# Kernel tuning notes

Measured on AMD Instinct MI355X. Metric: run time of the kernel, lower is better.

The kernel has to match this reference:

```python
import jax, jax.numpy as jnp
import numpy as np

TARGET_FIDELITY = 0.95
WEIGHT = 0.1
BATCH, DIM = 8192, 2048


def setup_inputs() -> dict:
    key = jax.random.key(0)
    k1, k2 = jax.random.split(key)
    # Scale by 1/sqrt(DIM) so each row is roughly unit-norm (quantum-state-like)
    # and the trace fidelity lands strictly inside the clamp interval [0, 1].
    scale = 1.0 / np.sqrt(DIM)
    latent_codes = jax.random.normal(k1, (BATCH, DIM), dtype=jnp.float32) * scale
    target_codes = jax.random.normal(k2, (BATCH, DIM), dtype=jnp.float32) * scale
    return {"latent_codes": latent_codes, "target_codes": target_codes}


def reference(latent_codes, target_codes):
    batch = latent_codes.shape[0]
    # rho = mean_i z_i z_i^T  ==  L^T L / B  (single GEMM instead of B outer products)
    rho = jnp.matmul(latent_codes.T, latent_codes) / batch      # [D, D]
    sigma = jnp.matmul(target_codes.T, target_codes) / batch    # [D, D]
    # trace(rho @ sigma) = sum(rho * sigma) since both are symmetric
    fidelity = jnp.clip(jnp.sum(rho * sigma), 0.0, 1.0)
    loss = WEIGHT * jnp.abs(fidelity - TARGET_FIDELITY)
    return loss
```

## Files before the change

kernel.cpp:

```cpp
#include <hip/hip_runtime.h>
#include <stdint.h>

#define BATCH 8192
#define DIM   2048

typedef unsigned char  u8;
typedef unsigned short u16;
typedef unsigned int   u32;

using v8i  = __attribute__((ext_vector_type(8)))  int;
using v16f = __attribute__((ext_vector_type(16))) float;

#if __has_builtin(__builtin_amdgcn_cvt_scalef32_pk_fp4_f32)
#define HW_FP4 1
#endif

__device__ __forceinline__ void gl_lds16(const void* g, void* l) {
  __builtin_amdgcn_global_load_lds(
      (const __attribute__((address_space(1))) u32*)g,
      (__attribute__((address_space(3))) u32*)l, 16, 0, 0);
}

__device__ __forceinline__ u32 nib4(float x) {
  float xs = x * 64.0f;
  float a  = fabsf(xs);
  u32 n = (u32)(a >= 0.25f) + (u32)(a >= 0.75f) + (u32)(a >= 1.25f) +
          (u32)(a >= 1.75f) + (u32)(a >= 2.5f)  + (u32)(a >= 3.5f)  +
          (u32)(a >= 5.0f);
  return n | (xs < 0.0f ? 8u : 0u);
}

__device__ __forceinline__ u16 pack4_fp4(float a, float b, float c, float d) {
#ifdef HW_FP4
  u32 w = __builtin_amdgcn_cvt_scalef32_pk_fp4_f32(0u,  a * 64.0f, b * 64.0f, 1.0f, 0);
  w     = __builtin_amdgcn_cvt_scalef32_pk_fp4_f32(w,   c * 64.0f, d * 64.0f, 1.0f, 1);
  return (u16)w;
#else
  return (u16)(nib4(a) | (nib4(b) << 4) | (nib4(c) << 8) | (nib4(d) << 12));
#endif
}

__global__ __launch_bounds__(256) void tcvt_fp4(
    const float* __restrict__ L, const float* __restrict__ T,
    u8* __restrict__ X, u8* __restrict__ Y,
    float* __restrict__ acc, u32* __restrict__ cnt)
{
  __shared__ u16 ls[64 * 68];

  const int tid = threadIdx.x;
  if (blockIdx.x == 0 && tid == 0) { *acc = 0.0f; *cnt = 0u; }

  int id = blockIdx.x;
  const float* src;
  u8* dst;
  if (id < 1024) { src = L; dst = X; }
  else           { src = T; dst = Y; id -= 1024; }
  const int d0 = (id & 31) * 64;
  const int b0 = (id >> 5) * 256;

  const int s  = tid & 15;
  const int g  = tid >> 4;
  const int sw = s & 12;

  float4 f[4][4];
#pragma unroll
  for (int j = 0; j < 4; ++j)
#pragma unroll
    for (int r = 0; r < 4; ++r)
      f[j][r] = *(const float4*)(src + (size_t)(b0 + j * 64 + g * 4 + r) * DIM
                                 + d0 + s * 4);

#pragma unroll
  for (int j = 0; j < 4; ++j) {
    const int w = (j * 16 + g) ^ sw;
    const float* fp[4] = {(const float*)&f[j][0], (const float*)&f[j][1],
                          (const float*)&f[j][2], (const float*)&f[j][3]};
#pragma unroll
    for (int i = 0; i < 4; ++i)
      ls[(s * 4 + i) * 68 + w] = pack4_fp4(fp[0][i], fp[1][i], fp[2][i], fp[3][i]);
  }
  __syncthreads();

#pragma unroll
  for (int j2 = 0; j2 < 2; ++j2) {
    const int d   = (tid >> 3) + j2 * 32;
    const int o8  = tid & 7;
    const int gsw = (d >> 4) & 3;
    const int g1  = (2 * o8)     ^ gsw;
    const int g2  = (2 * o8 + 1) ^ gsw;
    uint2 a = *(const uint2*)&ls[d * 68 + g1 * 4];
    uint2 b = *(const uint2*)&ls[d * 68 + g2 * 4];
    uint4 v = {a.x, a.y, b.x, b.y};
    *(uint4*)(dst + (size_t)(d0 + d) * (BATCH / 2) + (b0 >> 1) + o8 * 16) = v;
  }
}

__global__ __launch_bounds__(256, 2) void gram_fp4(
    const u8* __restrict__ X, const u8* __restrict__ Y,
    float* __restrict__ Gx, float* __restrict__ Gy)
{
  __shared__ u8 ls[2][2][16384];

  const int tid = threadIdx.x;
  const int bid = blockIdx.x;
  const int t   = bid & 255;
  const u8*  src = (bid < 256) ? X : Y;
  float*     dst = (bid < 256) ? Gx : Gy;
  const int i0  = (t >> 4) * 128;
  const int j0  = (t & 15) * 128;

  const int wave = tid >> 6;
  const int lane = tid & 63;
  const int wr = (wave >> 1) * 64;
  const int wc = (wave & 1) * 64;
  const int lr = lane & 31;
  const int kh = lane >> 5;

  u32 sdst[4], soi[4], soj[4];
#pragma unroll
  for (int rr = 0; rr < 4; ++rr) {
    const int li  = rr * 256 + tid;
    const int row = li >> 3;
    const int p   = li & 7;
    const int gc  = p ^ (row & 7);
    sdst[rr] = (u32)(row * 128 + p * 16);
    soi[rr]  = (u32)(i0 + row) * (BATCH / 2) + gc * 16;
    soj[rr]  = (u32)(j0 + row) * (BATCH / 2) + gc * 16;
  }

  u32 fa[2][4], fb[2][4];
#pragma unroll
  for (int h = 0; h < 2; ++h) {
    const int ra = wr + h * 32 + lr;
    const int rb = wc + h * 32 + lr;
#pragma unroll
    for (int ks = 0; ks < 4; ++ks) {
      const int c = 2 * ks + kh;
      fa[h][ks] = (u32)(ra * 128 + (c ^ (ra & 7)) * 16);
      fb[h][ks] = (u32)(rb * 128 + (c ^ (rb & 7)) * 16);
    }
  }

  v16f acc[2][2] = {};
  const int sc = 0x7F7F7F7F;

#pragma unroll
  for (int rr = 0; rr < 4; ++rr) {
    gl_lds16(src + soi[rr], &ls[0][0][sdst[rr]]);
    gl_lds16(src + soj[rr], &ls[0][1][sdst[rr]]);
  }

  for (int it = 0; it < 32; ++it) {
    __syncthreads();
    const int buf = it & 1;
    if (it < 31) {
      const u32 k1 = (u32)(it + 1) * 128;
#pragma unroll
      for (int rr = 0; rr < 4; ++rr) {
        gl_lds16(src + soi[rr] + k1, &ls[buf ^ 1][0][sdst[rr]]);
        gl_lds16(src + soj[rr] + k1, &ls[buf ^ 1][1][sdst[rr]]);
      }
    }
    const u8* pI = ls[buf][0];
    const u8* pJ = ls[buf][1];
#pragma unroll
    for (int ks = 0; ks < 4; ++ks) {
      v8i a[2], b[2];
#pragma unroll
      for (int h = 0; h < 2; ++h) {
        int4 pa = *(const int4*)&pI[fa[h][ks]];
        a[h] = (v8i){pa.x, pa.y, pa.z, pa.w, 0, 0, 0, 0};
        int4 pb = *(const int4*)&pJ[fb[h][ks]];
        b[h] = (v8i){pb.x, pb.y, pb.z, pb.w, 0, 0, 0, 0};
      }
#pragma unroll
      for (int h = 0; h < 2; ++h)
#pragma unroll
        for (int hc = 0; hc < 2; ++hc)
          acc[h][hc] = __builtin_amdgcn_mfma_scale_f32_32x32x64_f8f6f4(
              a[h], b[hc], acc[h][hc],  4,  4,
              0, sc, 0, sc);
    }
  }

  float4* o = (float4*)(dst + (size_t)t * 16384);
#pragma unroll
  for (int h = 0; h < 2; ++h)
#pragma unroll
    for (int hc = 0; hc < 2; ++hc)
#pragma unroll
      for (int r4 = 0; r4 < 4; ++r4) {
        float4 v = {acc[h][hc][r4 * 4 + 0], acc[h][hc][r4 * 4 + 1],
                    acc[h][hc][r4 * 4 + 2], acc[h][hc][r4 * 4 + 3]};
        o[((h * 2 + hc) * 4 + r4) * 256 + tid] = v;
      }
}

__global__ __launch_bounds__(256) void dot_kernel(
    const float4* __restrict__ Gx, const float4* __restrict__ Gy,
    float* __restrict__ d_acc, u32* __restrict__ d_cnt,
    float* __restrict__ out)
{
  __shared__ float red[4];
  const int tid  = threadIdx.x;
  const int lane = tid & 63;
  const int i0   = blockIdx.x * 256 + tid;
  float s = 0.0f;
#pragma unroll
  for (int j = 0; j < 4; ++j) {
    float4 a = Gx[i0 + j * 262144];
    float4 b = Gy[i0 + j * 262144];
    s += a.x * b.x + a.y * b.y + a.z * b.z + a.w * b.w;
  }
#pragma unroll
  for (int off = 32; off > 0; off >>= 1)
    s += __shfl_down(s, off);
  if (lane == 0) red[tid >> 6] = s;
  __syncthreads();
  if (tid == 0) {
    atomicAdd(d_acc, red[0] + red[1] + red[2] + red[3]);
    __threadfence();
    const u32 old = atomicAdd(d_cnt, 1u);
    if (old == 1023u) {
      float S   = atomicAdd(d_acc, 0.0f);
      float fid = S * 0x1.0p-50f;
      fid = fminf(fmaxf(fid, 0.0f), 1.0f);
      *out = 0.1f * fabsf(fid - 0.95f);
    }
  }
}

extern "C" void kernel_launch(void* const* d_in, const int* in_sizes, int n_in,
                              void* d_out, int out_size, void* d_ws, size_t ws_size,
                              hipStream_t stream) {
  const float* L = (const float*)d_in[0];
  const float* T = (const float*)d_in[1];
  float* out = (float*)d_out;

  const size_t NF4 = (size_t)BATCH * DIM / 2;
  const size_t GEL = (size_t)DIM * DIM;
  u8*    X   = (u8*)d_ws;
  u8*    Y   = (u8*)d_ws + NF4;
  float* Gx  = (float*)((char*)d_ws + 2 * NF4);
  float* Gy  = Gx + GEL;
  float* acc = Gy + GEL;
  u32*   cnt = (u32*)(acc + 1);

  tcvt_fp4<<<2048, 256, 0, stream>>>(L, T, X, Y, acc, cnt);
  gram_fp4<<<512, 256, 0, stream>>>(X, Y, Gx, Gy);
  dot_kernel<<<1024, 256, 0, stream>>>((const float4*)Gx, (const float4*)Gy,
                                       acc, cnt, out);
}
```

Before: 228.3 us.

## Exploit Gram symmetry with triangular tiles and stream-K split across blocks

Only the lower-triangular 128x128 tiles of each Gram matrix are computed: 136 per matrix, 272 in total. Their K iterations are spread evenly over 512 blocks, 17 quanta each, in stream-K style, and partial tiles are combined with float atomicAdd into a zeroed buffer. The dot kernel weights off-diagonal tiles by two, which roughly halves GEMM work and the Gram storage it reads. The costs are many scalar atomics per tile boundary, zeroing the buffer inside the convert kernel, and nondeterministic float summation order. The convert kernel also now double-buffers its input loads.

```diff
diff --git a/kernel.cpp b/kernel.cpp
--- a/kernel.cpp
+++ b/kernel.cpp
@@ -3,13 +3,17 @@
 
 #define BATCH 8192
 #define DIM   2048
+#define NT    272
+#define QTOT  (NT * 32)
+#define QPB   17
 
 typedef unsigned char  u8;
 typedef unsigned short u16;
 typedef unsigned int   u32;
 
-using v8i  = __attribute__((ext_vector_type(8)))  int;
-using v16f = __attribute__((ext_vector_type(16))) float;
+using v8i   = __attribute__((ext_vector_type(8)))  int;
+using v16f  = __attribute__((ext_vector_type(16))) float;
+using f32x4 = __attribute__((ext_vector_type(4)))  float;
 
 #if __has_builtin(__builtin_amdgcn_cvt_scalef32_pk_fp4_f32)
 #define HW_FP4 1
@@ -43,12 +47,18 @@
 __global__ __launch_bounds__(256) void tcvt_fp4(
     const float* __restrict__ L, const float* __restrict__ T,
     u8* __restrict__ X, u8* __restrict__ Y,
-    float* __restrict__ acc, u32* __restrict__ cnt)
+    float* __restrict__ Gc, float* __restrict__ acc, u32* __restrict__ cnt)
 {
   __shared__ u16 ls[64 * 68];
 
   const int tid = threadIdx.x;
   if (blockIdx.x == 0 && tid == 0) { *acc = 0.0f; *cnt = 0u; }
+
+  {
+    const float4 z = {0.f, 0.f, 0.f, 0.f};
+    for (int i = blockIdx.x * 256 + tid; i < NT * 4096; i += 2048 * 256)
+      ((float4*)Gc)[i] = z;
+  }
 
   int id = blockIdx.x;
   const float* src;
@@ -62,22 +72,25 @@
   const int g  = tid >> 4;
   const int sw = s & 12;
 
-  float4 f[4][4];
-#pragma unroll
-  for (int j = 0; j < 4; ++j)
-#pragma unroll
-    for (int r = 0; r < 4; ++r)
-      f[j][r] = *(const float4*)(src + (size_t)(b0 + j * 64 + g * 4 + r) * DIM
-                                 + d0 + s * 4);
+  const float* base = src + (size_t)(b0 + g * 4) * DIM + d0 + s * 4;
+
+  f32x4 f[2][4];
+#pragma unroll
+  for (int r = 0; r < 4; ++r)
+    f[0][r] = *(const f32x4*)(base + (size_t)r * DIM);
 
 #pragma unroll
   for (int j = 0; j < 4; ++j) {
+    if (j < 3) {
+#pragma unroll
+      for (int r = 0; r < 4; ++r)
+        f[(j + 1) & 1][r] = *(const f32x4*)(base + (size_t)((j + 1) * 64 + r) * DIM);
+    }
     const int w = (j * 16 + g) ^ sw;
-    const float* fp[4] = {(const float*)&f[j][0], (const float*)&f[j][1],
-                          (const float*)&f[j][2], (const float*)&f[j][3]};
 #pragma unroll
     for (int i = 0; i < 4; ++i)
-      ls[(s * 4 + i) * 68 + w] = pack4_fp4(fp[0][i], fp[1][i], fp[2][i], fp[3][i]);
+      ls[(s * 4 + i) * 68 + w] =
+          pack4_fp4(f[j & 1][0][i], f[j & 1][1][i], f[j & 1][2][i], f[j & 1][3][i]);
   }
   __syncthreads();
 
@@ -97,17 +110,12 @@
 
 __global__ __launch_bounds__(256, 2) void gram_fp4(
     const u8* __restrict__ X, const u8* __restrict__ Y,
-    float* __restrict__ Gx, float* __restrict__ Gy)
+    float* __restrict__ Gc)
 {
   __shared__ u8 ls[2][2][16384];
 
   const int tid = threadIdx.x;
   const int bid = blockIdx.x;
-  const int t   = bid & 255;
-  const u8*  src = (bid < 256) ? X : Y;
-  float*     dst = (bid < 256) ? Gx : Gy;
-  const int i0  = (t >> 4) * 128;
-  const int j0  = (t & 15) * 128;
 
   const int wave = tid >> 6;
   const int lane = tid & 63;
@@ -116,16 +124,15 @@
   const int lr = lane & 31;
   const int kh = lane >> 5;
 
-  u32 sdst[4], soi[4], soj[4];
+  u32 sdst[4]; int srow[4], sgc16[4];
 #pragma unroll
   for (int rr = 0; rr < 4; ++rr) {
     const int li  = rr * 256 + tid;
     const int row = li >> 3;
     const int p   = li & 7;
-    const int gc  = p ^ (row & 7);
-    sdst[rr] = (u32)(row * 128 + p * 16);
-    soi[rr]  = (u32)(i0 + row) * (BATCH / 2) + gc * 16;
-    soj[rr]  = (u32)(j0 + row) * (BATCH / 2) + gc * 16;
+    sdst[rr]  = (u32)(row * 128 + p * 16);
+    srow[rr]  = row;
+    sgc16[rr] = (p ^ (row & 7)) * 16;
   }
 
   u32 fa[2][4], fb[2][4];
@@ -144,23 +151,69 @@
   v16f acc[2][2] = {};
   const int sc = 0x7F7F7F7F;
 
-#pragma unroll
-  for (int rr = 0; rr < 4; ++rr) {
-    gl_lds16(src + soi[rr], &ls[0][0][sdst[rr]]);
-    gl_lds16(src + soj[rr], &ls[0][1][sdst[rr]]);
-  }
-
-  for (int it = 0; it < 32; ++it) {
+  const int q0 = bid * QPB;
+  int cur_t = -1, buf = 0;
+  const u8* src = X;
+  u32 soi[4], soj[4];
+
+  for (int it = 0; it < QPB; ++it) {
+    const int q = q0 + it;
+    const int t = q >> 5;
+    const int k = q & 31;
+
+    if (t != cur_t) {
+      if (cur_t >= 0) {
+        float* gt = Gc + (size_t)cur_t * 16384;
+#pragma unroll
+        for (int h = 0; h < 2; ++h)
+#pragma unroll
+          for (int hc = 0; hc < 2; ++hc)
+#pragma unroll
+            for (int r4 = 0; r4 < 4; ++r4) {
+              const int o = (((h * 2 + hc) * 4 + r4) * 256 + tid) * 4;
+#pragma unroll
+              for (int c2 = 0; c2 < 4; ++c2)
+                atomicAdd(gt + o + c2, acc[h][hc][r4 * 4 + c2]);
+            }
+#pragma unroll
+        for (int h = 0; h < 2; ++h)
+#pragma unroll
+          for (int hc = 0; hc < 2; ++hc)
+#pragma unroll
+            for (int c2 = 0; c2 < 16; ++c2)
+              acc[h][hc][c2] = 0.0f;
+      }
+      const int ltile = (t < 136) ? t : t - 136;
+      src = (t < 136) ? X : Y;
+      int ti = 0;
+      while ((ti + 1) * (ti + 2) / 2 <= ltile) ++ti;
+      const int tj = ltile - ti * (ti + 1) / 2;
+      const int i0 = ti * 128;
+      const int j0 = tj * 128;
+#pragma unroll
+      for (int rr = 0; rr < 4; ++rr) {
+        soi[rr] = (u32)(i0 + srow[rr]) * (BATCH / 2) + sgc16[rr];
+        soj[rr] = (u32)(j0 + srow[rr]) * (BATCH / 2) + sgc16[rr];
+      }
+      const u32 kb = (u32)k * 128;
+#pragma unroll
+      for (int rr = 0; rr < 4; ++rr) {
+        gl_lds16(src + soi[rr] + kb, &ls[buf][0][sdst[rr]]);
+        gl_lds16(src + soj[rr] + kb, &ls[buf][1][sdst[rr]]);
+      }
+      cur_t = t;
+    }
+
     __syncthreads();
-    const int buf = it & 1;
-    if (it < 31) {
-      const u32 k1 = (u32)(it + 1) * 128;
+    if (it + 1 < QPB && ((q + 1) >> 5) == t) {
+      const u32 kb = (u32)(k + 1) * 128;
 #pragma unroll
       for (int rr = 0; rr < 4; ++rr) {
-        gl_lds16(src + soi[rr] + k1, &ls[buf ^ 1][0][sdst[rr]]);
-        gl_lds16(src + soj[rr] + k1, &ls[buf ^ 1][1][sdst[rr]]);
-      }
-    }
+        gl_lds16(src + soi[rr] + kb, &ls[buf ^ 1][0][sdst[rr]]);
+        gl_lds16(src + soj[rr] + kb, &ls[buf ^ 1][1][sdst[rr]]);
+      }
+    }
+
     const u8* pI = ls[buf][0];
     const u8* pJ = ls[buf][1];
 #pragma unroll
@@ -181,37 +234,51 @@
               a[h], b[hc], acc[h][hc],  4,  4,
               0, sc, 0, sc);
     }
-  }
-
-  float4* o = (float4*)(dst + (size_t)t * 16384);
-#pragma unroll
-  for (int h = 0; h < 2; ++h)
-#pragma unroll
-    for (int hc = 0; hc < 2; ++hc)
-#pragma unroll
-      for (int r4 = 0; r4 < 4; ++r4) {
-        float4 v = {acc[h][hc][r4 * 4 + 0], acc[h][hc][r4 * 4 + 1],
-                    acc[h][hc][r4 * 4 + 2], acc[h][hc][r4 * 4 + 3]};
-        o[((h * 2 + hc) * 4 + r4) * 256 + tid] = v;
-      }
+    buf ^= 1;
+  }
+
+  {
+    float* gt = Gc + (size_t)cur_t * 16384;
+#pragma unroll
+    for (int h = 0; h < 2; ++h)
+#pragma unroll
+      for (int hc = 0; hc < 2; ++hc)
+#pragma unroll
+        for (int r4 = 0; r4 < 4; ++r4) {
+          const int o = (((h * 2 + hc) * 4 + r4) * 256 + tid) * 4;
+#pragma unroll
+          for (int c2 = 0; c2 < 4; ++c2)
+            atomicAdd(gt + o + c2, acc[h][hc][r4 * 4 + c2]);
+        }
+  }
 }
 
 __global__ __launch_bounds__(256) void dot_kernel(
-    const float4* __restrict__ Gx, const float4* __restrict__ Gy,
+    const float4* __restrict__ Gc4,
     float* __restrict__ d_acc, u32* __restrict__ d_cnt,
     float* __restrict__ out)
 {
   __shared__ float red[4];
   const int tid  = threadIdx.x;
   const int lane = tid & 63;
-  const int i0   = blockIdx.x * 256 + tid;
+  const int lt   = blockIdx.x >> 1;
+  const int half = blockIdx.x & 1;
+
+  int ti = 0;
+  while ((ti + 1) * (ti + 2) / 2 <= lt) ++ti;
+  const int tj = lt - ti * (ti + 1) / 2;
+  const float w = (ti == tj) ? 1.0f : 2.0f;
+
+  const float4* gx = Gc4 + (size_t)lt * 4096 + half * 2048;
+  const float4* gy = Gc4 + (size_t)(136 + lt) * 4096 + half * 2048;
   float s = 0.0f;
 #pragma unroll
-  for (int j = 0; j < 4; ++j) {
-    float4 a = Gx[i0 + j * 262144];
-    float4 b = Gy[i0 + j * 262144];
+  for (int j = 0; j < 8; ++j) {
+    float4 a = gx[tid + j * 256];
+    float4 b = gy[tid + j * 256];
     s += a.x * b.x + a.y * b.y + a.z * b.z + a.w * b.w;
   }
+  s *= w;
 #pragma unroll
   for (int off = 32; off > 0; off >>= 1)
     s += __shfl_down(s, off);
@@ -221,7 +288,7 @@
     atomicAdd(d_acc, red[0] + red[1] + red[2] + red[3]);
     __threadfence();
     const u32 old = atomicAdd(d_cnt, 1u);
-    if (old == 1023u) {
+    if (old == 271u) {
       float S   = atomicAdd(d_acc, 0.0f);
       float fid = S * 0x1.0p-50f;
       fid = fminf(fmaxf(fid, 0.0f), 1.0f);
@@ -238,16 +305,13 @@
   float* out = (float*)d_out;
 
   const size_t NF4 = (size_t)BATCH * DIM / 2;
-  const size_t GEL = (size_t)DIM * DIM;
   u8*    X   = (u8*)d_ws;
   u8*    Y   = (u8*)d_ws + NF4;
-  float* Gx  = (float*)((char*)d_ws + 2 * NF4);
-  float* Gy  = Gx + GEL;
-  float* acc = Gy + GEL;
+  float* Gc  = (float*)((char*)d_ws + 2 * NF4);
+  float* acc = Gc + (size_t)NT * 16384;
   u32*   cnt = (u32*)(acc + 1);
 
-  tcvt_fp4<<<2048, 256, 0, stream>>>(L, T, X, Y, acc, cnt);
-  gram_fp4<<<512, 256, 0, stream>>>(X, Y, Gx, Gy);
-  dot_kernel<<<1024, 256, 0, stream>>>((const float4*)Gx, (const float4*)Gy,
-                                       acc, cnt, out);
-}
+  tcvt_fp4<<<2048, 256, 0, stream>>>(L, T, X, Y, Gc, acc, cnt);
+  gram_fp4<<<512, 256, 0, stream>>>(X, Y, Gc);
+  dot_kernel<<<272, 256, 0, stream>>>((const float4*)Gc, acc, cnt, out);
+}
```

Result: slower. 324.1 us (+42.0%).
